# Optimization experiments

Hardware: AMD Instinct MI355X
Metric: run time of the kernel (lower is better)

The kernel has to match this reference:

```python
import jax, jax.numpy as jnp
import numpy as np

B, N, D = 4, 2048, 512
H, HD = 8, 64  # heads, output_dim per head


def setup_inputs() -> dict:
    key = jax.random.key(0)
    ks = jax.random.split(key, 6)
    x = jax.random.normal(ks[0], (B, N, D), dtype=jnp.float32)
    adj = (jax.random.uniform(ks[1], (N, N)) < 0.1).astype(jnp.float32)
    adj = jnp.maximum(adj, jnp.eye(N, dtype=jnp.float32))
    s = 0.02
    Wq = jax.random.normal(ks[2], (D, H * HD), dtype=jnp.float32) * s
    Wk = jax.random.normal(ks[3], (D, H * HD), dtype=jnp.float32) * s
    Wv = jax.random.normal(ks[4], (D, H * HD), dtype=jnp.float32) * s
    bq = jnp.zeros((H * HD,), dtype=jnp.float32)
    bk = jnp.zeros((H * HD,), dtype=jnp.float32)
    bv = jnp.zeros((H * HD,), dtype=jnp.float32)
    return {"x": x, "adj": adj, "Wq": Wq, "bq": bq, "Wk": Wk, "bk": bk, "Wv": Wv, "bv": bv}


def reference(x, adj, Wq, bq, Wk, bk, Wv, bv):
    b, n, _ = x.shape
    q = (x @ Wq + bq).reshape(b, n, H, HD)
    k = (x @ Wk + bk).reshape(b, n, H, HD)
    v = (x @ Wv + bv).reshape(b, n, H, HD)
    # scores: [b, h, i, j]
    scores = jnp.einsum('bihd,bjhd->bhij', q, k) / jnp.sqrt(jnp.float32(HD))
    mask = jnp.where(adj == 0, jnp.float32(-1e9), jnp.float32(0.0))  # [n, n]
    scores = scores + mask[None, None, :, :]
    weights = jax.nn.softmax(scores, axis=-1)
    # dropout is identity at inference (training=False)
    out = jnp.einsum('bhij,bjhd->bihd', weights, v)
    return out.reshape(b, n, H * HD)
```

## Files before the change

kernel.cpp:

```cpp
#include <hip/hip_runtime.h>
#include <hip/hip_bf16.h>
#include <stdint.h>

#define NTOK 2048
#define DIN  512
#define QSCALE 0.18033688011112042f

typedef __attribute__((ext_vector_type(8))) short bf16x8;
typedef __attribute__((ext_vector_type(4))) short bf16x4;
typedef __attribute__((ext_vector_type(4))) float f32x4;

#define MFMA16(a, b, c) __builtin_amdgcn_mfma_f32_16x16x32_bf16((a), (b), (c), 0, 0, 0)

union u4bf8 { uint4 u; bf16x8 h; };

static __device__ __forceinline__ short f2bf(float f) {
  union { float f; uint32_t u; } v; v.f = f;
  uint32_t r = (v.u + 0x7FFFu + ((v.u >> 16) & 1u)) >> 16;
  return (short)r;
}

__global__ __launch_bounds__(256) void k_xbf(const float* __restrict__ x, short* __restrict__ xb) {
  size_t i = (size_t)blockIdx.x * 256 + threadIdx.x;
  const float4 v = *(const float4*)(x + i * 4);
  bf16x4 h;
  h[0] = f2bf(v.x); h[1] = f2bf(v.y); h[2] = f2bf(v.z); h[3] = f2bf(v.w);
  *(bf16x4*)(xb + i * 4) = h;
}

__global__ __launch_bounds__(256) void k_wt(const float* __restrict__ W, short* __restrict__ Wt) {
  __shared__ float tile[32][33];
  int bo = blockIdx.x * 32, bc = blockIdx.y * 32;
  int tx = threadIdx.x & 31, ty = threadIdx.x >> 5;
#pragma unroll
  for (int q = 0; q < 4; ++q)
    tile[ty + q * 8][tx] = W[(bc + ty + q * 8) * DIN + bo + tx];
  __syncthreads();
#pragma unroll
  for (int q = 0; q < 4; ++q)
    Wt[(bo + ty + q * 8) * DIN + bc + tx] = f2bf(tile[tx][ty + q * 8]);
}

__global__ __launch_bounds__(256) void k_mask(const float* __restrict__ adj,
                                              unsigned long long* __restrict__ m64) {
  int wid = ((blockIdx.x * blockDim.x + threadIdx.x) >> 6);
  int lane = threadIdx.x & 63;
  int i = wid >> 5, wd = wid & 31;
  float a = adj[i * NTOK + wd * 64 + lane];
  unsigned long long b = __ballot(a != 0.0f);
  if (lane == 0) m64[i * 32 + wd] = b;
}

__global__ __launch_bounds__(256) void k_qkv(const short* __restrict__ xb,
                                             const short* __restrict__ Wt,
                                             const float* __restrict__ bq,
                                             const float* __restrict__ bk,
                                             const float* __restrict__ bv,
                                             short* __restrict__ Qb, short* __restrict__ Kb,
                                             short* __restrict__ Vb) {
  __shared__ short As[128 * 40];
  __shared__ short Bs[128 * 40];
  const int z = blockIdx.z;
  const short* Wz = Wt + z * DIN * DIN;
  const float* bias = (z == 0) ? bq : ((z == 1) ? bk : bv);
  const int mbase = blockIdx.x * 128, nbase = blockIdx.y * 128;
  const int tid = threadIdx.x;
  const int lane = tid & 63, w = tid >> 6;
  const int wr = w >> 1, wc = w & 1;
  const int lrow = lane & 15, lgrp = lane >> 4;

  f32x4 acc[4][4];
#pragma unroll
  for (int a = 0; a < 4; ++a)
#pragma unroll
    for (int b = 0; b < 4; ++b) acc[a][b] = (f32x4){0.f, 0.f, 0.f, 0.f};

  for (int kb = 0; kb < DIN; kb += 32) {
#pragma unroll
    for (int t = 0; t < 2; ++t) {
      int idx = tid + t * 256;
      int r = idx >> 2, c8 = idx & 3;
      *(bf16x8*)(As + r * 40 + c8 * 8) =
          *(const bf16x8*)(xb + (size_t)(mbase + r) * DIN + kb + c8 * 8);
    }
#pragma unroll
    for (int t = 0; t < 2; ++t) {
      int idx = tid + t * 256;
      int r = idx >> 2, c8 = idx & 3;
      *(bf16x8*)(Bs + r * 40 + c8 * 8) =
          *(const bf16x8*)(Wz + (size_t)(nbase + r) * DIN + kb + c8 * 8);
    }
    __syncthreads();
    bf16x8 af[4], bf[4];
#pragma unroll
    for (int mi = 0; mi < 4; ++mi)
      af[mi] = *(bf16x8*)(As + (wr * 64 + mi * 16 + lrow) * 40 + lgrp * 8);
#pragma unroll
    for (int ni = 0; ni < 4; ++ni)
      bf[ni] = *(bf16x8*)(Bs + (wc * 64 + ni * 16 + lrow) * 40 + lgrp * 8);
#pragma unroll
    for (int mi = 0; mi < 4; ++mi)
#pragma unroll
      for (int ni = 0; ni < 4; ++ni) acc[mi][ni] = MFMA16(af[mi], bf[ni], acc[mi][ni]);
    __syncthreads();
  }

#pragma unroll
  for (int ni = 0; ni < 4; ++ni) {
    int go = nbase + wc * 64 + ni * 16 + lrow;
    float bv_ = bias[go];
    int h = go >> 6, d = go & 63;
#pragma unroll
    for (int mi = 0; mi < 4; ++mi) {
#pragma unroll
      for (int v = 0; v < 4; ++v) {
        int gm = mbase + wr * 64 + mi * 16 + lgrp * 4 + v;
        int b = gm >> 11, n = gm & 2047;
        int bh = b * 8 + h;
        float val = acc[mi][ni][v] + bv_;
        if (z == 0)
          Qb[(size_t)bh * (NTOK * 64) + n * 64 + d] = f2bf(val * QSCALE);
        else if (z == 1)
          Kb[(size_t)bh * (NTOK * 64) + n * 64 + d] = f2bf(val);
        else
          Vb[(size_t)bh * (64 * NTOK) + d * NTOK + n] = f2bf(val);
      }
    }
  }
}

__global__ __launch_bounds__(256, 3) void k_attn(const short* __restrict__ Qb,
                                                 const short* __restrict__ Kb,
                                                 const short* __restrict__ Vb,
                                                 const unsigned long long* __restrict__ m64,
                                                 float* __restrict__ out) {
  __shared__ char smem[18432];
  short* Kl = (short*)smem;
  short* Vl = (short*)(smem + 9216);
  f32x4* ored = (f32x4*)smem;
  float* lsum = (float*)(smem + 16384);

  const int itile = blockIdx.x, bh = blockIdx.y;
  const int ibase = itile * 64;
  const int tid = threadIdx.x, lane = tid & 63, w = tid >> 6;
  const int wi = w >> 1, wj = w & 1;
  const int lrow = lane & 15, lgrp = lane >> 4;

  const short* Qp = Qb + (size_t)bh * (NTOK * 64);
  const short* Kp = Kb + (size_t)bh * (NTOK * 64);
  const short* Vp = Vb + (size_t)bh * (64 * NTOK);

  bf16x8 qa[2][2];
  const unsigned long long* mword[2];
#pragma unroll
  for (int ig = 0; ig < 2; ++ig) {
    const int qrow = ibase + wi * 32 + ig * 16 + lrow;
    qa[ig][0] = *(const bf16x8*)(Qp + (size_t)qrow * 64 + lgrp * 8);
    qa[ig][1] = *(const bf16x8*)(Qp + (size_t)qrow * 64 + 32 + lgrp * 8);
    mword[ig] = m64 + (size_t)qrow * 32;
  }

  const int r0 = tid >> 3, s0 = tid & 7;

  f32x4 oacc[2][4];
#pragma unroll
  for (int ig = 0; ig < 2; ++ig)
#pragma unroll
    for (int dn = 0; dn < 4; ++dn) oacc[ig][dn] = (f32x4){0.f, 0.f, 0.f, 0.f};
  float lrun[2] = {0.f, 0.f};

  uint4 pfK0 = *(const uint4*)(Kp + (size_t)r0 * 64 + s0 * 8);
  uint4 pfK1 = *(const uint4*)(Kp + (size_t)(r0 + 32) * 64 + s0 * 8);
  uint4 pfV0 = *(const uint4*)(Vp + (size_t)r0 * NTOK + s0 * 8);
  uint4 pfV1 = *(const uint4*)(Vp + (size_t)(r0 + 32) * NTOK + s0 * 8);
  unsigned long long mw[2] = {mword[0][0], mword[1][0]};
  *(uint4*)(Kl + r0 * 72 + s0 * 8) = pfK0;
  *(uint4*)(Kl + (r0 + 32) * 72 + s0 * 8) = pfK1;
  *(uint4*)(Vl + r0 * 72 + s0 * 8) = pfV0;
  *(uint4*)(Vl + (r0 + 32) * 72 + s0 * 8) = pfV1;
  __syncthreads();

  for (int jt = 0; jt < 32; ++jt) {
    unsigned long long mwn[2] = {0ull, 0ull};
    if (jt < 31) {
      const int jn = (jt + 1) * 64;
      pfK0 = *(const uint4*)(Kp + (size_t)(jn + r0) * 64 + s0 * 8);
      pfK1 = *(const uint4*)(Kp + (size_t)(jn + r0 + 32) * 64 + s0 * 8);
      pfV0 = *(const uint4*)(Vp + (size_t)r0 * NTOK + jn + s0 * 8);
      pfV1 = *(const uint4*)(Vp + (size_t)(r0 + 32) * NTOK + jn + s0 * 8);
      mwn[0] = mword[0][jt + 1];
      mwn[1] = mword[1][jt + 1];
    }

    uint32_t pk[2][2][2];
#pragma unroll
    for (int jsub = 0; jsub < 2; ++jsub) {
      const int krow = (wj * 32 + jsub * 16 + lrow) * 72;
      bf16x8 kf0 = *(bf16x8*)(Kl + krow + lgrp * 8);
      bf16x8 kf1 = *(bf16x8*)(Kl + krow + 32 + lgrp * 8);
#pragma unroll
      for (int ig = 0; ig < 2; ++ig) {
        f32x4 zz = (f32x4){0.f, 0.f, 0.f, 0.f};
        zz = MFMA16(kf0, qa[ig][0], zz);
        zz = MFMA16(kf1, qa[ig][1], zz);
        const uint32_t bits = (uint32_t)(mw[ig] >> (wj * 32 + jsub * 16 + lgrp * 4));
        float p0 = (bits & 1u) ? exp2f(zz[0]) : 0.f;
        float p1 = (bits & 2u) ? exp2f(zz[1]) : 0.f;
        float p2 = (bits & 4u) ? exp2f(zz[2]) : 0.f;
        float p3 = (bits & 8u) ? exp2f(zz[3]) : 0.f;
        lrun[ig] += (p0 + p1) + (p2 + p3);
        uint32_t w0, w1;
        asm("v_cvt_pk_bf16_f32 %0, %1, %2" : "=v"(w0) : "v"(p0), "v"(p1));
        asm("v_cvt_pk_bf16_f32 %0, %1, %2" : "=v"(w1) : "v"(p2), "v"(p3));
        pk[ig][jsub][0] = w0;
        pk[ig][jsub][1] = w1;
      }
    }

#pragma unroll
    for (int dn = 0; dn < 4; ++dn) {
      const int vrow = (dn * 16 + lrow) * 72 + wj * 32 + lgrp * 4;
      const uint2 v0 = *(const uint2*)(Vl + vrow);
      const uint2 v1 = *(const uint2*)(Vl + vrow + 16);
      u4bf8 vb;
      vb.u = (uint4){v0.x, v0.y, v1.x, v1.y};
#pragma unroll
      for (int ig = 0; ig < 2; ++ig) {
        u4bf8 pa;
        pa.u = (uint4){pk[ig][0][0], pk[ig][0][1], pk[ig][1][0], pk[ig][1][1]};
        oacc[ig][dn] = MFMA16(pa.h, vb.h, oacc[ig][dn]);
      }
    }

    if (jt < 31) {
      __syncthreads();
      *(uint4*)(Kl + r0 * 72 + s0 * 8) = pfK0;
      *(uint4*)(Kl + (r0 + 32) * 72 + s0 * 8) = pfK1;
      *(uint4*)(Vl + r0 * 72 + s0 * 8) = pfV0;
      *(uint4*)(Vl + (r0 + 32) * 72 + s0 * 8) = pfV1;
      mw[0] = mwn[0];
      mw[1] = mwn[1];
      __syncthreads();
    }
  }

  __syncthreads();

#pragma unroll
  for (int ig = 0; ig < 2; ++ig) {
    float s = lrun[ig];
    s += __shfl_xor(s, 16);
    s += __shfl_xor(s, 32);
    if (lane < 16) lsum[(w * 2 + ig) * 16 + lane] = s;
  }
  if (wj == 1) {
#pragma unroll
    for (int ig = 0; ig < 2; ++ig)
#pragma unroll
      for (int dn = 0; dn < 4; ++dn)
        ored[((wi * 2 + ig) * 4 + dn) * 64 + lane] = oacc[ig][dn];
  }
  __syncthreads();

  if (wj == 0) {
    const int b = bh >> 3, h = bh & 7;
#pragma unroll
    for (int ig = 0; ig < 2; ++ig) {
      const f32x4 la = *(const f32x4*)&lsum[((wi * 2 + 0) * 2 + ig) * 16 + lgrp * 4];
      const f32x4 lb = *(const f32x4*)&lsum[((wi * 2 + 1) * 2 + ig) * 16 + lgrp * 4];
      float inv[4];
#pragma unroll
      for (int v = 0; v < 4; ++v) inv[v] = 1.0f / (la[v] + lb[v]);
#pragma unroll
      for (int dn = 0; dn < 4; ++dn) {
        f32x4 s = oacc[ig][dn] + ored[((wi * 2 + ig) * 4 + dn) * 64 + lane];
#pragma unroll
        for (int v = 0; v < 4; ++v) {
          int i = ibase + wi * 32 + ig * 16 + lgrp * 4 + v;
          out[(size_t)(b * NTOK + i) * DIN + h * 64 + dn * 16 + lrow] = s[v] * inv[v];
        }
      }
    }
  }
}

extern "C" void kernel_launch(void* const* d_in, const int* in_sizes, int n_in,
                              void* d_out, int out_size, void* d_ws, size_t ws_size,
                              hipStream_t stream) {
  const float* x   = (const float*)d_in[0];
  const float* adj = (const float*)d_in[1];
  const float* Wq  = (const float*)d_in[2];
  const float* bq  = (const float*)d_in[3];
  const float* Wk  = (const float*)d_in[4];
  const float* bk  = (const float*)d_in[5];
  const float* Wv  = (const float*)d_in[6];
  const float* bv  = (const float*)d_in[7];
  float* out = (float*)d_out;

  char* ws = (char*)d_ws;
  short* Qb = (short*)(ws);
  short* Kb = (short*)(ws + (8u << 20));
  short* Vb = (short*)(ws + (16u << 20));
  short* Wt = (short*)(ws + (24u << 20));
  unsigned long long* m64 = (unsigned long long*)(ws + (26u << 20));
  short* xb = (short*)d_out;

  k_xbf<<<4096, 256, 0, stream>>>(x, xb);
  k_wt<<<dim3(16, 16), 256, 0, stream>>>(Wq, Wt);
  k_wt<<<dim3(16, 16), 256, 0, stream>>>(Wk, Wt + 262144);
  k_wt<<<dim3(16, 16), 256, 0, stream>>>(Wv, Wt + 524288);
  k_mask<<<16384, 256, 0, stream>>>(adj, m64);
  k_qkv<<<dim3(64, 4, 3), 256, 0, stream>>>(xb, Wt, bq, bk, bv, Qb, Kb, Vb);
  k_attn<<<dim3(32, 32), 256, 0, stream>>>(Qb, Kb, Vb, m64, out);
}
```

Baseline: 129.5 us.

## Double-buffer LDS tiles in QKV GEMM and attention, merge weight transposes

The QKV projection GEMM now uses two LDS buffers with register prefetch of the next K-slice, so each iteration needs one barrier instead of two. The attention kernel likewise double-buffers its K/V tiles, which removes the barrier before the next tile is written. The three weight-transpose launches are merged into a single 3D-grid launch. In exchange, attention LDS use doubles to 36 KB per block, which may reduce occupancy, and the GEMM carries more prefetch registers under a new occupancy hint.

```diff
diff --git a/kernel.cpp b/kernel.cpp
--- a/kernel.cpp
+++ b/kernel.cpp
@@ -28,7 +28,12 @@
   *(bf16x4*)(xb + i * 4) = h;
 }
 
-__global__ __launch_bounds__(256) void k_wt(const float* __restrict__ W, short* __restrict__ Wt) {
+__global__ __launch_bounds__(256) void k_wt(const float* __restrict__ Wq,
+                                            const float* __restrict__ Wk,
+                                            const float* __restrict__ Wv,
+                                            short* __restrict__ Wt) {
+  const float* W = (blockIdx.z == 0) ? Wq : ((blockIdx.z == 1) ? Wk : Wv);
+  short* Wo = Wt + (size_t)blockIdx.z * DIN * DIN;
   __shared__ float tile[32][33];
   int bo = blockIdx.x * 32, bc = blockIdx.y * 32;
   int tx = threadIdx.x & 31, ty = threadIdx.x >> 5;
@@ -38,7 +43,7 @@
   __syncthreads();
 #pragma unroll
   for (int q = 0; q < 4; ++q)
-    Wt[(bo + ty + q * 8) * DIN + bc + tx] = f2bf(tile[tx][ty + q * 8]);
+    Wo[(bo + ty + q * 8) * DIN + bc + tx] = f2bf(tile[tx][ty + q * 8]);
 }
 
 __global__ __launch_bounds__(256) void k_mask(const float* __restrict__ adj,
@@ -51,15 +56,15 @@
   if (lane == 0) m64[i * 32 + wd] = b;
 }
 
-__global__ __launch_bounds__(256) void k_qkv(const short* __restrict__ xb,
-                                             const short* __restrict__ Wt,
-                                             const float* __restrict__ bq,
-                                             const float* __restrict__ bk,
-                                             const float* __restrict__ bv,
-                                             short* __restrict__ Qb, short* __restrict__ Kb,
-                                             short* __restrict__ Vb) {
-  __shared__ short As[128 * 40];
-  __shared__ short Bs[128 * 40];
+__global__ __launch_bounds__(256, 3) void k_qkv(const short* __restrict__ xb,
+                                                const short* __restrict__ Wt,
+                                                const float* __restrict__ bq,
+                                                const float* __restrict__ bk,
+                                                const float* __restrict__ bv,
+                                                short* __restrict__ Qb, short* __restrict__ Kb,
+                                                short* __restrict__ Vb) {
+  __shared__ short As[2][128 * 40];
+  __shared__ short Bs[2][128 * 40];
   const int z = blockIdx.z;
   const short* Wz = Wt + z * DIN * DIN;
   const float* bias = (z == 0) ? bq : ((z == 1) ? bk : bv);
@@ -68,6 +73,7 @@
   const int lane = tid & 63, w = tid >> 6;
   const int wr = w >> 1, wc = w & 1;
   const int lrow = lane & 15, lgrp = lane >> 4;
+  const int ra = tid >> 2, ca = tid & 3;
 
   f32x4 acc[4][4];
 #pragma unroll
@@ -75,34 +81,49 @@
 #pragma unroll
     for (int b = 0; b < 4; ++b) acc[a][b] = (f32x4){0.f, 0.f, 0.f, 0.f};
 
-  for (int kb = 0; kb < DIN; kb += 32) {
-#pragma unroll
-    for (int t = 0; t < 2; ++t) {
-      int idx = tid + t * 256;
-      int r = idx >> 2, c8 = idx & 3;
-      *(bf16x8*)(As + r * 40 + c8 * 8) =
-          *(const bf16x8*)(xb + (size_t)(mbase + r) * DIN + kb + c8 * 8);
-    }
-#pragma unroll
-    for (int t = 0; t < 2; ++t) {
-      int idx = tid + t * 256;
-      int r = idx >> 2, c8 = idx & 3;
-      *(bf16x8*)(Bs + r * 40 + c8 * 8) =
-          *(const bf16x8*)(Wz + (size_t)(nbase + r) * DIN + kb + c8 * 8);
-    }
-    __syncthreads();
+  uint4 pA[2], pB[2];
+#pragma unroll
+  for (int u = 0; u < 2; ++u) {
+    pA[u] = *(const uint4*)(xb + (size_t)(mbase + ra + u * 64) * DIN + ca * 8);
+    pB[u] = *(const uint4*)(Wz + (size_t)(nbase + ra + u * 64) * DIN + ca * 8);
+  }
+#pragma unroll
+  for (int u = 0; u < 2; ++u) {
+    *(uint4*)(&As[0][(ra + u * 64) * 40 + ca * 8]) = pA[u];
+    *(uint4*)(&Bs[0][(ra + u * 64) * 40 + ca * 8]) = pB[u];
+  }
+  __syncthreads();
+
+  for (int t = 0; t < 16; ++t) {
+    const int cur = t & 1, nxt = cur ^ 1;
+    if (t < 15) {
+      const int kb = (t + 1) * 32;
+#pragma unroll
+      for (int u = 0; u < 2; ++u) {
+        pA[u] = *(const uint4*)(xb + (size_t)(mbase + ra + u * 64) * DIN + kb + ca * 8);
+        pB[u] = *(const uint4*)(Wz + (size_t)(nbase + ra + u * 64) * DIN + kb + ca * 8);
+      }
+    }
     bf16x8 af[4], bf[4];
 #pragma unroll
     for (int mi = 0; mi < 4; ++mi)
-      af[mi] = *(bf16x8*)(As + (wr * 64 + mi * 16 + lrow) * 40 + lgrp * 8);
+      af[mi] = *(bf16x8*)(&As[cur][(wr * 64 + mi * 16 + lrow) * 40 + lgrp * 8]);
 #pragma unroll
     for (int ni = 0; ni < 4; ++ni)
-      bf[ni] = *(bf16x8*)(Bs + (wc * 64 + ni * 16 + lrow) * 40 + lgrp * 8);
+      bf[ni] = *(bf16x8*)(&Bs[cur][(wc * 64 + ni * 16 + lrow) * 40 + lgrp * 8]);
 #pragma unroll
     for (int mi = 0; mi < 4; ++mi)
 #pragma unroll
       for (int ni = 0; ni < 4; ++ni) acc[mi][ni] = MFMA16(af[mi], bf[ni], acc[mi][ni]);
-    __syncthreads();
+
+    if (t < 15) {
+#pragma unroll
+      for (int u = 0; u < 2; ++u) {
+        *(uint4*)(&As[nxt][(ra + u * 64) * 40 + ca * 8]) = pA[u];
+        *(uint4*)(&Bs[nxt][(ra + u * 64) * 40 + ca * 8]) = pB[u];
+      }
+      __syncthreads();
+    }
   }
 
 #pragma unroll
@@ -134,9 +155,7 @@
                                                  const short* __restrict__ Vb,
                                                  const unsigned long long* __restrict__ m64,
                                                  float* __restrict__ out) {
-  __shared__ char smem[18432];
-  short* Kl = (short*)smem;
-  short* Vl = (short*)(smem + 9216);
+  __shared__ char smem[36864];
   f32x4* ored = (f32x4*)smem;
   float* lsum = (float*)(smem + 16384);
 
@@ -174,13 +193,19 @@
   uint4 pfV0 = *(const uint4*)(Vp + (size_t)r0 * NTOK + s0 * 8);
   uint4 pfV1 = *(const uint4*)(Vp + (size_t)(r0 + 32) * NTOK + s0 * 8);
   unsigned long long mw[2] = {mword[0][0], mword[1][0]};
-  *(uint4*)(Kl + r0 * 72 + s0 * 8) = pfK0;
-  *(uint4*)(Kl + (r0 + 32) * 72 + s0 * 8) = pfK1;
-  *(uint4*)(Vl + r0 * 72 + s0 * 8) = pfV0;
-  *(uint4*)(Vl + (r0 + 32) * 72 + s0 * 8) = pfV1;
+  {
+    short* Kl0 = (short*)smem;
+    short* Vl0 = (short*)(smem + 9216);
+    *(uint4*)(Kl0 + r0 * 72 + s0 * 8) = pfK0;
+    *(uint4*)(Kl0 + (r0 + 32) * 72 + s0 * 8) = pfK1;
+    *(uint4*)(Vl0 + r0 * 72 + s0 * 8) = pfV0;
+    *(uint4*)(Vl0 + (r0 + 32) * 72 + s0 * 8) = pfV1;
+  }
   __syncthreads();
 
   for (int jt = 0; jt < 32; ++jt) {
+    short* KlC = (short*)(smem + (jt & 1) * 18432);
+    short* VlC = (short*)(smem + (jt & 1) * 18432 + 9216);
     unsigned long long mwn[2] = {0ull, 0ull};
     if (jt < 31) {
       const int jn = (jt + 1) * 64;
@@ -196,8 +221,8 @@
 #pragma unroll
     for (int jsub = 0; jsub < 2; ++jsub) {
       const int krow = (wj * 32 + jsub * 16 + lrow) * 72;
-      bf16x8 kf0 = *(bf16x8*)(Kl + krow + lgrp * 8);
-      bf16x8 kf1 = *(bf16x8*)(Kl + krow + 32 + lgrp * 8);
+      bf16x8 kf0 = *(bf16x8*)(KlC + krow + lgrp * 8);
+      bf16x8 kf1 = *(bf16x8*)(KlC + krow + 32 + lgrp * 8);
 #pragma unroll
       for (int ig = 0; ig < 2; ++ig) {
         f32x4 zz = (f32x4){0.f, 0.f, 0.f, 0.f};
@@ -220,8 +245,8 @@
 #pragma unroll
     for (int dn = 0; dn < 4; ++dn) {
       const int vrow = (dn * 16 + lrow) * 72 + wj * 32 + lgrp * 4;
-      const uint2 v0 = *(const uint2*)(Vl + vrow);
-      const uint2 v1 = *(const uint2*)(Vl + vrow + 16);
+      const uint2 v0 = *(const uint2*)(VlC + vrow);
+      const uint2 v1 = *(const uint2*)(VlC + vrow + 16);
       u4bf8 vb;
       vb.u = (uint4){v0.x, v0.y, v1.x, v1.y};
 #pragma unroll
@@ -233,11 +258,12 @@
     }
 
     if (jt < 31) {
-      __syncthreads();
-      *(uint4*)(Kl + r0 * 72 + s0 * 8) = pfK0;
-      *(uint4*)(Kl + (r0 + 32) * 72 + s0 * 8) = pfK1;
-      *(uint4*)(Vl + r0 * 72 + s0 * 8) = pfV0;
-      *(uint4*)(Vl + (r0 + 32) * 72 + s0 * 8) = pfV1;
+      short* KlN = (short*)(smem + ((jt + 1) & 1) * 18432);
+      short* VlN = (short*)(smem + ((jt + 1) & 1) * 18432 + 9216);
+      *(uint4*)(KlN + r0 * 72 + s0 * 8) = pfK0;
+      *(uint4*)(KlN + (r0 + 32) * 72 + s0 * 8) = pfK1;
+      *(uint4*)(VlN + r0 * 72 + s0 * 8) = pfV0;
+      *(uint4*)(VlN + (r0 + 32) * 72 + s0 * 8) = pfV1;
       mw[0] = mwn[0];
       mw[1] = mwn[1];
       __syncthreads();
@@ -306,9 +332,7 @@
   short* xb = (short*)d_out;
 
   k_xbf<<<4096, 256, 0, stream>>>(x, xb);
-  k_wt<<<dim3(16, 16), 256, 0, stream>>>(Wq, Wt);
-  k_wt<<<dim3(16, 16), 256, 0, stream>>>(Wk, Wt + 262144);
-  k_wt<<<dim3(16, 16), 256, 0, stream>>>(Wv, Wt + 524288);
+  k_wt<<<dim3(16, 16, 3), 256, 0, stream>>>(Wq, Wk, Wv, Wt);
   k_mask<<<16384, 256, 0, stream>>>(adj, m64);
   k_qkv<<<dim3(64, 4, 3), 256, 0, stream>>>(xb, Wt, bq, bk, bv, Qb, Kb, Vb);
   k_attn<<<dim3(32, 32), 256, 0, stream>>>(Qb, Kb, Vb, m64, out);
```

After: 120.7 us. -6.8%, faster.
